# Performance work log

Hardware: AMD Instinct MI355X
Metric: run time of the kernel (lower is better)

## Reference

```python
import jax, jax.numpy as jnp
import numpy as np

G = 9.80665  # scipy.constants.g


def _xavier(key, fan_in, fan_out):
    std = np.sqrt(2.0 / (fan_in + fan_out))
    return jax.random.normal(key, (fan_in, fan_out), dtype=jnp.float32) * std


def setup_inputs() -> dict:
    key = jax.random.key(0)
    ks = jax.random.split(key, 16)
    n_samples, n_nodes, n_pipes, n_demand, hidden = 16384, 512, 1024, 256, 64
    D = jax.random.uniform(ks[0], (n_samples, n_demand), dtype=jnp.float32) * 0.01
    leak_id = jax.random.randint(ks[1], (n_samples, 1), 0, n_pipes)
    A0 = jax.random.normal(ks[2], (n_nodes, n_pipes), dtype=jnp.float32) * 0.1
    inv = jax.random.normal(ks[3], (n_nodes, n_pipes), dtype=jnp.float32) * 0.1
    M = jax.random.normal(ks[4], (n_nodes, n_pipes), dtype=jnp.float32) * 0.1
    supply = jax.random.uniform(ks[5], (n_pipes,), dtype=jnp.float32) * 10.0
    L = jax.random.uniform(ks[6], (n_pipes,), dtype=jnp.float32) * 900.0 + 100.0  # pipe length [m]
    d = jax.random.uniform(ks[7], (n_pipes,), dtype=jnp.float32) * 0.4 + 0.1      # diameter [m]
    C = jax.random.uniform(ks[8], (n_pipes,), dtype=jnp.float32) * 50.0 + 100.0   # HW coefficient
    demand_idx = jnp.arange(n_demand) * 2  # distinct node indices < n_nodes
    a = jnp.float32(0.01)   # leak area
    Cd = jnp.float32(0.75)  # discharge coefficient
    W1 = _xavier(ks[9], 1, hidden); b1 = jnp.zeros((hidden,), jnp.float32)
    W2 = _xavier(ks[10], hidden, hidden); b2 = jnp.zeros((hidden,), jnp.float32)
    W3 = _xavier(ks[11], hidden, 1); b3 = jnp.zeros((1,), jnp.float32)
    base = jax.random.normal(ks[12], (n_pipes,), dtype=jnp.float32) * 0.1
    return {"D": D, "leak_id": leak_id, "A0": A0, "inv": inv, "M": M,
            "supply": supply, "L": L, "d": d, "C": C, "a": a, "Cd": Cd,
            "W1": W1, "b1": b1, "W2": W2, "b2": b2, "W3": W3, "b3": b3,
            "base": base, "demand_idx": demand_idx}


def reference(D, leak_id, A0, inv, M, supply, L, d, C, a, Cd,
              W1, b1, W2, b2, W3, b3, base, demand_idx):
    S = D.shape[0]
    n_nodes, n_pipes = M.shape
    idx = leak_id[:, 0]  # [S] int, pipe index per sample

    # Net(leak_id): tanh MLP + lookup of per-pipe base value
    x = leak_id.astype(jnp.float32)                      # [S,1]
    h = jnp.tanh(x @ W1 + b1)
    h = jnp.tanh(h @ W2 + b2)
    net_out = base[idx][:, None] + (h @ W3 + b3)          # [S,1]

    # scatter-built demand / leakage / areas
    demand = jnp.zeros((S, n_nodes), jnp.float32).at[:, demand_idx].set(D)
    rows = jnp.arange(S)
    leakage = jnp.zeros((S, n_pipes), jnp.float32).at[rows, idx].set(net_out[:, 0])
    areas = jnp.zeros((S, n_pipes), jnp.float32).at[rows, idx].set(a)

    # q = inv.T @ (M @ leakage + demand)
    y = jnp.einsum('np,sp->sn', M, leakage) + demand      # [S,Nn]
    q = jnp.einsum('np,sn->sp', inv, y)                   # [S,Np]

    # Hazen-Williams head loss
    hL = jnp.sign(q) * 10.667 * C[None] ** (-1.852) * d[None] ** (-4.871) * L[None] * jnp.abs(q) ** 1.852
    H = jnp.einsum('np,sp->sn', inv, supply[None] - hL)   # [S,Nn]

    # leak demand d_leak = Cd * (M @ areas) * sqrt(2 g relu(H))  (safe sqrt)
    Hp = jax.nn.relu(H)
    sq = jnp.sqrt(jnp.where(Hp > 0, Hp, 1.0)) * (Hp > 0).astype(jnp.float32)
    d_leak = Cd * jnp.einsum('np,sp->sn', M, areas) * jnp.sqrt(jnp.float32(2.0 * G)) * sq

    residual = jnp.einsum('np,sp->sn', A0, q) - demand - d_leak
    return jnp.mean(residual ** 2)
```

## Files before the change

kernel.cpp:

```cpp
#include <hip/hip_runtime.h>
#include <math.h>

typedef _Float16 f16;
typedef _Float16 f16x4 __attribute__((ext_vector_type(4)));
typedef _Float16 f16x8 __attribute__((ext_vector_type(8)));
typedef float f32x4 __attribute__((ext_vector_type(4)));

#define S_TOTAL 16384
#define N_NODES 512
#define N_PIPES 1024
#define N_DEM   256
#define HIDDEN  64
#define T_SCALE 256.0f

#define GLOAD16(gsrc, ldst) \
    __builtin_amdgcn_global_load_lds((const __attribute__((address_space(1))) void*)(gsrc), \
                                     (__attribute__((address_space(3))) void*)(ldst), 16, 0, 0)
#define SBAR()  __builtin_amdgcn_s_barrier()
#define FENCE() asm volatile("" ::: "memory")
#define WAITN(n) asm volatile("s_waitcnt vmcnt(" #n ")" ::: "memory")

__global__ __launch_bounds__(256) void prep_all(
    const float* __restrict__ W1, const float* __restrict__ b1,
    const float* __restrict__ W2, const float* __restrict__ b2,
    const float* __restrict__ W3, const float* __restrict__ b3,
    const float* __restrict__ base,
    const float* __restrict__ L, const float* __restrict__ dpipe,
    const float* __restrict__ Cw,
    const float* __restrict__ Mf, const float* __restrict__ inv,
    const float* __restrict__ A0, const float* __restrict__ D,
    const int* __restrict__ dmap,
    float* __restrict__ net, float* __restrict__ lKc,
    f16* __restrict__ MT16, f16* __restrict__ invT16,
    f16* __restrict__ inv16, f16* __restrict__ A016, f16* __restrict__ D16,
    f16* __restrict__ DI16, f16* __restrict__ IDXT,
    float* __restrict__ out, int out_size)
{
    __shared__ __align__(16) f16 tile[64][72];
    const int b = blockIdx.x, t = threadIdx.x;
    if (b < 256) {
        if (b == 0) for (int i = t; i < out_size; i += 256) out[i] = 0.f;
        const int wid = t >> 6, k = t & 63;
        const int p = b * 4 + wid;
        const float x = (float)p;
        float h1 = tanhf(x * W1[k] + b1[k]);
        float acc = b2[k];
        #pragma unroll
        for (int j = 0; j < HIDDEN; ++j) {
            float hj = __shfl(h1, j, 64);
            acc = fmaf(hj, W2[j * HIDDEN + k], acc);
        }
        float partial = tanhf(acc) * W3[k];
        #pragma unroll
        for (int off = 32; off > 0; off >>= 1) partial += __shfl_down(partial, off, 64);
        if (k == 0) {
            net[p] = base[p] + partial + b3[0];
            lKc[p] = log2f(10.667f) - 1.852f * log2f(Cw[p]) - 4.871f * log2f(dpipe[p]) + log2f(L[p]);
        }
        return;
    }
    if (b < 512) {
        const int idx = b - 256;
        const float* in = (idx < 128) ? Mf : inv;
        f16* outp = (idx < 128) ? MT16 : invT16;
        const int i2 = idx & 127;
        const int bx = i2 & 15, by = i2 >> 4;
        const int r0 = by * 64, c0 = bx * 64;
        const int lr = t / 16, lc4 = (t % 16) * 4;
        #pragma unroll
        for (int i = 0; i < 4; ++i) {
            int r = lr + i * 16;
            float4 v = *(const float4*)(in + (size_t)(r0 + r) * N_PIPES + c0 + lc4);
            tile[lc4 + 0][r] = (f16)v.x; tile[lc4 + 1][r] = (f16)v.y;
            tile[lc4 + 2][r] = (f16)v.z; tile[lc4 + 3][r] = (f16)v.w;
        }
        __syncthreads();
        const int wrow = t / 4, wc16 = (t % 4) * 16;
        *(f16x8*)(outp + (size_t)(c0 + wrow) * N_NODES + r0 + wc16)     = *(f16x8*)&tile[wrow][wc16];
        *(f16x8*)(outp + (size_t)(c0 + wrow) * N_NODES + r0 + wc16 + 8) = *(f16x8*)&tile[wrow][wc16 + 8];
        return;
    }
    const int tid = (b - 512) * 256 + t;
    const int np = 768 * 256;
    for (int i = tid; i < (N_NODES * N_PIPES) / 4; i += np) {
        float4 v = ((const float4*)inv)[i];
        ((f16x4*)inv16)[i] = (f16x4){(f16)v.x, (f16)v.y, (f16)v.z, (f16)v.w};
        float4 w = ((const float4*)A0)[i];
        ((f16x4*)A016)[i] = (f16x4){(f16)w.x, (f16)w.y, (f16)w.z, (f16)w.w};
    }
    for (int i = tid; i < (S_TOTAL * N_DEM) / 4; i += np) {
        float4 v = ((const float4*)D)[i];
        ((f16x4*)D16)[i] = (f16x4){(f16)v.x, (f16)v.y, (f16)v.z, (f16)v.w};
    }
    for (int i = tid; i < N_DEM * (N_PIPES / 4); i += np) {
        int j = i >> 8, p0 = (i & 255) * 4;
        float4 v = *(const float4*)(inv + (size_t)dmap[j] * N_PIPES + p0);
        *(f16x4*)(DI16 + (size_t)j * N_PIPES + p0) = (f16x4){(f16)v.x, (f16)v.y, (f16)v.z, (f16)v.w};
    }
    for (int i = tid; i < N_PIPES * (N_DEM / 4); i += np) {
        int p = i >> 6, j0 = (i & 63) * 4;
        f16x4 o;
        #pragma unroll
        for (int u = 0; u < 4; ++u)
            o[u] = (f16)inv[(size_t)dmap[j0 + u] * N_PIPES + p];
        *(f16x4*)(IDXT + (size_t)p * N_DEM + j0) = o;
    }
}

struct GemmP {
    const f16* A; int lda;
    const f16* B; int ldb;
    f16* C; int ldc;
    int K;
    const int* dmap;
    int gx, gy;
};

__device__ __forceinline__ void gemm_body(const GemmP& P, int bx, int by) {
    __shared__ __align__(16) f16 As[128][72], Bs[64][72];
    const int m0 = by * 128, c0 = bx * 64;
    const int t = threadIdx.x, lane = t & 63, wid = t >> 6;
    const int wr = wid >> 1, wc = wid & 1;
    const int cl = lane & 15, g = lane >> 4;
    const int tr = t >> 3, tc = (t & 7) * 8;
    f32x4 acc[4][2] = {};
    for (int k0 = 0; k0 < P.K; k0 += 64) {
        #pragma unroll
        for (int r = 0; r < 4; ++r) {
            int row = r * 32 + tr;
            *(f16x8*)&As[row][tc] = *(const f16x8*)(P.A + (size_t)(m0 + row) * P.lda + k0 + tc);
        }
        #pragma unroll
        for (int r = 0; r < 2; ++r) {
            int row = r * 32 + tr;
            *(f16x8*)&Bs[row][tc] = *(const f16x8*)(P.B + (size_t)(c0 + row) * P.ldb + k0 + tc);
        }
        __syncthreads();
        #pragma unroll
        for (int kk = 0; kk < 2; ++kk) {
            const int kb = kk * 32 + g * 8;
            f16x8 a[4], bfr[2];
            #pragma unroll
            for (int m = 0; m < 4; ++m) a[m] = *(const f16x8*)&As[wr * 64 + m * 16 + cl][kb];
            #pragma unroll
            for (int n = 0; n < 2; ++n) bfr[n] = *(const f16x8*)&Bs[wc * 32 + n * 16 + cl][kb];
            #pragma unroll
            for (int m = 0; m < 4; ++m)
                #pragma unroll
                for (int n = 0; n < 2; ++n)
                    acc[m][n] = __builtin_amdgcn_mfma_f32_16x16x32_f16(a[m], bfr[n], acc[m][n], 0, 0, 0);
        }
        __syncthreads();
    }
    #pragma unroll
    for (int m = 0; m < 4; ++m)
        #pragma unroll
        for (int reg = 0; reg < 4; ++reg) {
            const int row = m0 + wr * 64 + m * 16 + g * 4 + reg;
            #pragma unroll
            for (int n = 0; n < 2; ++n) {
                const int col = c0 + wc * 32 + n * 16 + cl;
                float v = acc[m][n][reg];
                if (P.dmap && P.dmap[col] == row) v -= 1.0f;
                P.C[(size_t)row * P.ldc + col] = (f16)v;
            }
        }
}

__global__ __launch_bounds__(256) void gemm_small3(GemmP p0, GemmP p1, GemmP p2) {
    const GemmP& P = (blockIdx.z == 0) ? p0 : (blockIdx.z == 1) ? p1 : p2;
    if ((int)blockIdx.x >= P.gx || (int)blockIdx.y >= P.gy) return;
    gemm_body(P, blockIdx.x, blockIdx.y);
}

__global__ __launch_bounds__(512, 4) void gemm_qt_mfma(
    const f16* __restrict__ D16, const int* __restrict__ leak_id,
    const f16* __restrict__ IDXT, const float* __restrict__ net,
    const f16* __restrict__ G16, const float* __restrict__ lKc,
    const float* __restrict__ supply, f16* __restrict__ t16,
    const f16* __restrict__ MT16, const f16* __restrict__ Wt,
    f16* __restrict__ G2out)
{
    __shared__ __align__(16) f16 As[2][128][64];
    __shared__ __align__(16) f16 Bs[2][128][64];
    const int t = threadIdx.x, lane = t & 63, wid = t >> 6;

    if (blockIdx.y >= 128) {
        f16 (*A2)[72] = (f16(*)[72])&Bs[0][0][0];
        f16 (*B2)[72] = (f16(*)[72])&As[0][0][0];
        const int m0 = ((int)blockIdx.y - 128) * 128, c0 = blockIdx.x * 64;
        const int wr = wid >> 2, wc = wid & 3;
        const int cl = lane & 15, g = lane >> 4;
        f32x4 acc[4] = {};
        for (int k0 = 0; k0 < 512; k0 += 64) {
            {
                int r = t >> 2, c16 = (t & 3) * 16;
                *(f16x8*)&A2[r][c16]     = *(const f16x8*)(MT16 + (size_t)(m0 + r) * N_NODES + k0 + c16);
                *(f16x8*)&A2[r][c16 + 8] = *(const f16x8*)(MT16 + (size_t)(m0 + r) * N_NODES + k0 + c16 + 8);
                int r2 = t >> 3, c8 = (t & 7) * 8;
                *(f16x8*)&B2[r2][c8] = *(const f16x8*)(Wt + (size_t)(c0 + r2) * N_NODES + k0 + c8);
            }
            __syncthreads();
            #pragma unroll
            for (int kk = 0; kk < 2; ++kk) {
                const int kb = kk * 32 + g * 8;
                f16x8 b = *(const f16x8*)&B2[wc * 16 + cl][kb];
                #pragma unroll
                for (int m = 0; m < 4; ++m) {
                    f16x8 a = *(const f16x8*)&A2[wr * 64 + m * 16 + cl][kb];
                    acc[m] = __builtin_amdgcn_mfma_f32_16x16x32_f16(a, b, acc[m], 0, 0, 0);
                }
            }
            __syncthreads();
        }
        #pragma unroll
        for (int m = 0; m < 4; ++m)
            #pragma unroll
            for (int reg = 0; reg < 4; ++reg)
                G2out[(size_t)(m0 + wr * 64 + m * 16 + g * 4 + reg) * N_NODES + c0 + wc * 16 + cl] = (f16)acc[m][reg];
        return;
    }
    const int bid = blockIdx.y * 8 + blockIdx.x;
    const int w = (bid & 7) * 128 + (bid >> 3);
    const int bx = w & 7, by = w >> 3;
    const int p0 = bx * 128, sb = by * 128;
    const int wr = wid >> 2, wc = wid & 3;
    const int cl = lane & 15, g = lane >> 4;
    const int swrow = lane >> 3;
    const int swcol = ((lane & 7) ^ swrow) * 8;
    const int sx0 = (g ^ (cl & 7)) * 8, sx1 = ((4 + g) ^ (cl & 7)) * 8;

    const f16* Abase = D16 + (size_t)(sb + swrow) * N_DEM + swcol;
    const f16* Bbase = IDXT + (size_t)(p0 + swrow) * N_DEM + swcol;

    f32x4 acc[4][2] = {};
    auto stage = [&](int buf, int k0) {
        #pragma unroll
        for (int c = 0; c < 2; ++c) {
            int r0 = c * 64 + wid * 8;
            GLOAD16(Abase + (size_t)r0 * N_DEM + k0, &As[buf][r0][0]);
        }
        #pragma unroll
        for (int c = 0; c < 2; ++c) {
            int r0 = c * 64 + wid * 8;
            GLOAD16(Bbase + (size_t)r0 * N_DEM + k0, &Bs[buf][r0][0]);
        }
    };
    auto compute = [&](int buf) {
        #pragma unroll
        for (int kk = 0; kk < 2; ++kk) {
            const int sx = kk ? sx1 : sx0;
            f16x8 a[4], b[2];
            #pragma unroll
            for (int m = 0; m < 4; ++m) a[m] = *(const f16x8*)&As[buf][wr * 64 + m * 16 + cl][sx];
            #pragma unroll
            for (int n = 0; n < 2; ++n) b[n] = *(const f16x8*)&Bs[buf][wc * 32 + n * 16 + cl][sx];
            #pragma unroll
            for (int m = 0; m < 4; ++m)
                #pragma unroll
                for (int n = 0; n < 2; ++n)
                    acc[m][n] = __builtin_amdgcn_mfma_f32_16x16x32_f16(a[m], b[n], acc[m][n], 0, 0, 0);
        }
    };

    int cur = 0;
    stage(0, 0);
    #pragma unroll 1
    for (int k = 0; k < 3; ++k) {
        stage(cur ^ 1, (k + 1) * 64);
        WAITN(4); SBAR();
        compute(cur);
        FENCE(); SBAR();
        cur ^= 1;
    }
    WAITN(0); SBAR();
    compute(cur);

    float lKc2[2], sup2[2]; int pcol[2];
    #pragma unroll
    for (int n = 0; n < 2; ++n) {
        pcol[n] = p0 + wc * 32 + n * 16 + cl;
        lKc2[n] = lKc[pcol[n]]; sup2[n] = supply[pcol[n]];
    }
    #pragma unroll
    for (int m = 0; m < 4; ++m) {
        #pragma unroll
        for (int reg = 0; reg < 4; ++reg) {
            const int srow = sb + wr * 64 + m * 16 + g * 4 + reg;
            const int idx = leak_id[srow];
            const float nv = net[idx];
            #pragma unroll
            for (int n = 0; n < 2; ++n) {
                float qv = acc[m][n][reg] + nv * (float)G16[(size_t)idx * N_PIPES + pcol[n]];
                float l = __builtin_amdgcn_logf(fabsf(qv));
                float hL = copysignf(__builtin_amdgcn_exp2f(fmaf(1.852f, l, lKc2[n])), qv);
                t16[(size_t)srow * N_PIPES + pcol[n]] = (f16)((sup2[n] - hL) * (1.0f / T_SCALE));
            }
        }
    }
}

__global__ __launch_bounds__(512, 4) void gemm_res_mfma(
    const f16* __restrict__ t16, const f16* __restrict__ inv16,
    const f16* __restrict__ D16, const f16* __restrict__ P1p,
    const f16* __restrict__ MT16, const f16* __restrict__ G2_16,
    const int* __restrict__ leak_id, const float* __restrict__ net,
    const float* __restrict__ Cd_p, const float* __restrict__ a_p,
    float scale, float* __restrict__ out)
{
    __shared__ __align__(16) f16 As[2][128][64];
    __shared__ __align__(16) f16 Bs[2][128][64];
    const int nwg = gridDim.x * gridDim.y;
    const int bid = blockIdx.y * gridDim.x + blockIdx.x;
    const int w = (bid & 7) * (nwg >> 3) + (bid >> 3);
    const int bx = w % gridDim.x, by = w / gridDim.x;
    const int n0 = bx * 128, sb = by * 128;
    const int t = threadIdx.x, lane = t & 63, wid = t >> 6;
    const int wr = wid >> 2, wc = wid & 3;
    const int cl = lane & 15, g = lane >> 4;
    const int swrow = lane >> 3;
    const int swcol = ((lane & 7) ^ swrow) * 8;
    const int sx0 = (g ^ (cl & 7)) * 8, sx1 = ((4 + g) ^ (cl & 7)) * 8;

    const f16* HAb = t16   + (size_t)(sb + swrow) * N_PIPES + swcol;
    const f16* HBb = inv16 + (size_t)(n0 + swrow) * N_PIPES + swcol;
    const f16* RAb = D16   + (size_t)(sb + swrow) * N_DEM + swcol;
    const f16* RBb = P1p   + (size_t)(n0 + swrow) * N_DEM + swcol;

    f32x4 accH[4][2] = {}, accR[4][2] = {};

    auto stageH = [&](int buf, int k0) {
        #pragma unroll
        for (int c = 0; c < 2; ++c) {
            int r0 = c * 64 + wid * 8;
            GLOAD16(HAb + (size_t)r0 * N_PIPES + k0, &As[buf][r0][0]);
        }
        #pragma unroll
        for (int c = 0; c < 2; ++c) {
            int r0 = c * 64 + wid * 8;
            GLOAD16(HBb + (size_t)r0 * N_PIPES + k0, &Bs[buf][r0][0]);
        }
    };
    auto stageR = [&](int buf, int k0) {
        #pragma unroll
        for (int c = 0; c < 2; ++c) {
            int r0 = c * 64 + wid * 8;
            GLOAD16(RAb + (size_t)r0 * N_DEM + k0, &As[buf][r0][0]);
        }
        #pragma unroll
        for (int c = 0; c < 2; ++c) {
            int r0 = c * 64 + wid * 8;
            GLOAD16(RBb + (size_t)r0 * N_DEM + k0, &Bs[buf][r0][0]);
        }
    };
    auto computeT = [&](int buf, f32x4 (&accA)[4][2]) {
        #pragma unroll
        for (int kk = 0; kk < 2; ++kk) {
            const int sx = kk ? sx1 : sx0;
            f16x8 a[4], b[2];
            #pragma unroll
            for (int m = 0; m < 4; ++m) a[m] = *(const f16x8*)&As[buf][wr * 64 + m * 16 + cl][sx];
            #pragma unroll
            for (int n = 0; n < 2; ++n) b[n] = *(const f16x8*)&Bs[buf][wc * 32 + n * 16 + cl][sx];
            #pragma unroll
            for (int m = 0; m < 4; ++m)
                #pragma unroll
                for (int n = 0; n < 2; ++n)
                    accA[m][n] = __builtin_amdgcn_mfma_f32_16x16x32_f16(a[m], b[n], accA[m][n], 0, 0, 0);
        }
    };

    int cur = 0;
    stageH(0, 0);
    #pragma unroll 1
    for (int k = 0; k < 15; ++k) {
        stageH(cur ^ 1, (k + 1) * 64);
        WAITN(4); SBAR();
        computeT(cur, accH);
        FENCE(); SBAR();
        cur ^= 1;
    }
    stageR(cur ^ 1, 0);
    WAITN(4); SBAR();
    computeT(cur, accH);
    FENCE(); SBAR();
    cur ^= 1;
    #pragma unroll 1
    for (int k = 0; k < 3; ++k) {
        stageR(cur ^ 1, (k + 1) * 64);
        WAITN(4); SBAR();
        computeT(cur, accR);
        FENCE(); SBAR();
        cur ^= 1;
    }
    WAITN(0); SBAR();
    computeT(cur, accR);

    const float cda = Cd_p[0] * a_p[0] * sqrtf(2.f * 9.80665f);
    int node[2];
    #pragma unroll
    for (int n = 0; n < 2; ++n) node[n] = n0 + wc * 32 + n * 16 + cl;
    float lsum = 0.f;
    #pragma unroll
    for (int m = 0; m < 4; ++m) {
        #pragma unroll
        for (int reg = 0; reg < 4; ++reg) {
            const int srow = sb + wr * 64 + m * 16 + g * 4 + reg;
            const int idx = leak_id[srow];
            const float nv = net[idx];
            #pragma unroll
            for (int n = 0; n < 2; ++n) {
                const float H = accH[m][n][reg] * T_SCALE;
                const float sq = (H > 0.f) ? sqrtf(H) : 0.f;
                const float dl = cda * (float)MT16[(size_t)idx * N_NODES + node[n]] * sq;
                const float r = accR[m][n][reg] + nv * (float)G2_16[(size_t)idx * N_NODES + node[n]] - dl;
                lsum += r * r;
            }
        }
    }
    #pragma unroll
    for (int off = 32; off > 0; off >>= 1) lsum += __shfl_down(lsum, off, 64);
    __syncthreads();
    float* wred = (float*)&As[0][0][0];
    if (lane == 0) wred[wid] = lsum;
    __syncthreads();
    if (t == 0) {
        float tot = 0.f;
        #pragma unroll
        for (int i = 0; i < 8; ++i) tot += wred[i];
        atomicAdd(out, tot * scale);
    }
}

extern "C" void kernel_launch(void* const* d_in, const int* in_sizes, int n_in,
                              void* d_out, int out_size, void* d_ws, size_t ws_size,
                              hipStream_t stream) {
    const float* D          = (const float*)d_in[0];
    const int*   leak_id    = (const int*)  d_in[1];
    const float* A0         = (const float*)d_in[2];
    const float* inv        = (const float*)d_in[3];
    const float* M          = (const float*)d_in[4];
    const float* supply     = (const float*)d_in[5];
    const float* L          = (const float*)d_in[6];
    const float* dpipe      = (const float*)d_in[7];
    const float* C          = (const float*)d_in[8];
    const float* a_p        = (const float*)d_in[9];
    const float* Cd_p       = (const float*)d_in[10];
    const float* W1         = (const float*)d_in[11];
    const float* b1         = (const float*)d_in[12];
    const float* W2         = (const float*)d_in[13];
    const float* b2         = (const float*)d_in[14];
    const float* W3         = (const float*)d_in[15];
    const float* b3         = (const float*)d_in[16];
    const float* base       = (const float*)d_in[17];
    const int*   demand_idx = (const int*)  d_in[18];

    char* ws = (char*)d_ws;
    size_t off = 0;
    auto carve = [&](size_t bytes) { char* p = ws + off; off += (bytes + 255) & ~(size_t)255; return p; };
    float* net    = (float*)carve(N_PIPES * 4);
    float* lKc    = (float*)carve(N_PIPES * 4);
    f16* inv16  = (f16*)carve((size_t)N_NODES * N_PIPES * 2);
    f16* A016   = (f16*)carve((size_t)N_NODES * N_PIPES * 2);
    f16* MT16   = (f16*)carve((size_t)N_PIPES * N_NODES * 2);
    f16* invT16 = (f16*)carve((size_t)N_PIPES * N_NODES * 2);
    f16* G16    = (f16*)carve((size_t)N_PIPES * N_PIPES * 2);
    f16* G2_16  = (f16*)carve((size_t)N_PIPES * N_NODES * 2);
    f16* Wt     = (f16*)carve((size_t)N_NODES * N_NODES * 2);
    f16* P1p    = (f16*)carve((size_t)N_NODES * N_DEM * 2);
    f16* DI16   = (f16*)carve((size_t)N_DEM * N_PIPES * 2);
    f16* IDXT   = (f16*)carve((size_t)N_PIPES * N_DEM * 2);
    f16* D16    = (f16*)carve((size_t)S_TOTAL * N_DEM * 2);
    f16* t16    = (f16*)carve((size_t)S_TOTAL * N_PIPES * 2);

    prep_all<<<1280, 256, 0, stream>>>(
        W1, b1, W2, b2, W3, b3, base, L, dpipe, C,
        M, inv, A0, D, demand_idx,
        net, lKc, MT16, invT16, inv16, A016, D16, DI16, IDXT,
        (float*)d_out, out_size);

    GemmP pG16 = {MT16, N_NODES, invT16, N_NODES, G16, N_PIPES, N_NODES, nullptr, 16, 8};
    GemmP pWt  = {A016, N_PIPES, inv16, N_PIPES, Wt, N_NODES, N_PIPES, nullptr, 8, 4};
    GemmP pP1  = {A016, N_PIPES, DI16, N_PIPES, P1p, N_DEM, N_PIPES, demand_idx, 4, 4};
    gemm_small3<<<dim3(16, 8, 3), 256, 0, stream>>>(pG16, pWt, pP1);

    gemm_qt_mfma<<<dim3(8, 136), 512, 0, stream>>>(
        D16, leak_id, IDXT, net, G16, lKc, supply, t16, MT16, Wt, G2_16);

    const float scale = 1.f / ((float)S_TOTAL * (float)N_NODES);
    gemm_res_mfma<<<dim3(N_NODES / 128, S_TOTAL / 128), 512, 0, stream>>>(
        t16, inv16, D16, P1p, MT16, G2_16, leak_id, net, Cd_p, a_p,
        scale, (float*)d_out);
}
```

Measured before the change: 94.47 us.

## Store head-loss intermediate and inv in bf8 and use bf8 MFMA for H GEMM

The per-sample head-loss tensor t and the inv matrix are now quantized to 8-bit bf8 (e5m2) instead of f16. The H GEMM in the residual kernel uses 16x16x32 bf8 MFMA with 128-wide K tiles and a new LDS swizzle, halving the number of K iterations. This halves the bytes written and read for the large S x N_pipes intermediate and doubles MFMA throughput. The cost is a large loss of precision (2-bit mantissa) in H, which risks exceeding the correctness tolerance.

```diff
diff --git a/kernel.cpp b/kernel.cpp
--- a/kernel.cpp
+++ b/kernel.cpp
@@ -19,6 +19,12 @@
 #define SBAR()  __builtin_amdgcn_s_barrier()
 #define FENCE() asm volatile("" ::: "memory")
 #define WAITN(n) asm volatile("s_waitcnt vmcnt(" #n ")" ::: "memory")
+
+__device__ __forceinline__ unsigned char f32_to_bf8(float x) {
+    unsigned short h = __builtin_bit_cast(unsigned short, (f16)x);
+    unsigned short r = (unsigned short)(h + 0x7F + ((h >> 8) & 1));
+    return (unsigned char)(r >> 8);
+}
 
 __global__ __launch_bounds__(256) void prep_all(
     const float* __restrict__ W1, const float* __restrict__ b1,
@@ -32,7 +38,8 @@
     const int* __restrict__ dmap,
     float* __restrict__ net, float* __restrict__ lKc,
     f16* __restrict__ MT16, f16* __restrict__ invT16,
-    f16* __restrict__ inv16, f16* __restrict__ A016, f16* __restrict__ D16,
+    f16* __restrict__ inv16, unsigned char* __restrict__ inv8,
+    f16* __restrict__ A016, f16* __restrict__ D16,
     f16* __restrict__ DI16, f16* __restrict__ IDXT,
     float* __restrict__ out, int out_size)
 {
@@ -85,6 +92,8 @@
     for (int i = tid; i < (N_NODES * N_PIPES) / 4; i += np) {
         float4 v = ((const float4*)inv)[i];
         ((f16x4*)inv16)[i] = (f16x4){(f16)v.x, (f16)v.y, (f16)v.z, (f16)v.w};
+        uchar4 v8 = {f32_to_bf8(v.x), f32_to_bf8(v.y), f32_to_bf8(v.z), f32_to_bf8(v.w)};
+        ((uchar4*)inv8)[i] = v8;
         float4 w = ((const float4*)A0)[i];
         ((f16x4*)A016)[i] = (f16x4){(f16)w.x, (f16)w.y, (f16)w.z, (f16)w.w};
     }
@@ -177,7 +186,7 @@
     const f16* __restrict__ D16, const int* __restrict__ leak_id,
     const f16* __restrict__ IDXT, const float* __restrict__ net,
     const f16* __restrict__ G16, const float* __restrict__ lKc,
-    const float* __restrict__ supply, f16* __restrict__ t16,
+    const float* __restrict__ supply, unsigned char* __restrict__ t8,
     const f16* __restrict__ MT16, const f16* __restrict__ Wt,
     f16* __restrict__ G2out)
 {
@@ -294,22 +303,22 @@
                 float qv = acc[m][n][reg] + nv * (float)G16[(size_t)idx * N_PIPES + pcol[n]];
                 float l = __builtin_amdgcn_logf(fabsf(qv));
                 float hL = copysignf(__builtin_amdgcn_exp2f(fmaf(1.852f, l, lKc2[n])), qv);
-                t16[(size_t)srow * N_PIPES + pcol[n]] = (f16)((sup2[n] - hL) * (1.0f / T_SCALE));
+                t8[(size_t)srow * N_PIPES + pcol[n]] = f32_to_bf8((sup2[n] - hL) * (1.0f / T_SCALE));
             }
         }
     }
 }
 
 __global__ __launch_bounds__(512, 4) void gemm_res_mfma(
-    const f16* __restrict__ t16, const f16* __restrict__ inv16,
+    const unsigned char* __restrict__ t8, const unsigned char* __restrict__ inv8,
     const f16* __restrict__ D16, const f16* __restrict__ P1p,
     const f16* __restrict__ MT16, const f16* __restrict__ G2_16,
     const int* __restrict__ leak_id, const float* __restrict__ net,
     const float* __restrict__ Cd_p, const float* __restrict__ a_p,
     float scale, float* __restrict__ out)
 {
-    __shared__ __align__(16) f16 As[2][128][64];
-    __shared__ __align__(16) f16 Bs[2][128][64];
+    __shared__ __align__(16) unsigned char AsM[2][128 * 128];
+    __shared__ __align__(16) unsigned char BsM[2][128 * 128];
     const int nwg = gridDim.x * gridDim.y;
     const int bid = blockIdx.y * gridDim.x + blockIdx.x;
     const int w = (bid & 7) * (nwg >> 3) + (bid >> 3);
@@ -319,82 +328,103 @@
     const int wr = wid >> 2, wc = wid & 3;
     const int cl = lane & 15, g = lane >> 4;
     const int swrow = lane >> 3;
-    const int swcol = ((lane & 7) ^ swrow) * 8;
-    const int sx0 = (g ^ (cl & 7)) * 8, sx1 = ((4 + g) ^ (cl & 7)) * 8;
-
-    const f16* HAb = t16   + (size_t)(sb + swrow) * N_PIPES + swcol;
-    const f16* HBb = inv16 + (size_t)(n0 + swrow) * N_PIPES + swcol;
-    const f16* RAb = D16   + (size_t)(sb + swrow) * N_DEM + swcol;
-    const f16* RBb = P1p   + (size_t)(n0 + swrow) * N_DEM + swcol;
+    const int swb = ((lane & 7) ^ swrow) * 16;
+
+    const unsigned char* HAb = t8   + (size_t)(sb + swrow) * N_PIPES + swb;
+    const unsigned char* HBb = inv8 + (size_t)(n0 + swrow) * N_PIPES + swb;
+    const f16* RAb = D16 + (size_t)(sb + swrow) * N_DEM + swb / 2;
+    const f16* RBb = P1p + (size_t)(n0 + swrow) * N_DEM + swb / 2;
 
     f32x4 accH[4][2] = {}, accR[4][2] = {};
 
     auto stageH = [&](int buf, int k0) {
+        #pragma unroll
+        for (int c = 0; c < 2; ++c) {
+            int r0 = wid * 16 + c * 8;
+            GLOAD16(HAb + (size_t)r0 * N_PIPES + k0, &AsM[buf][r0 * 128]);
+        }
+        #pragma unroll
+        for (int c = 0; c < 2; ++c) {
+            int r0 = wid * 16 + c * 8;
+            GLOAD16(HBb + (size_t)r0 * N_PIPES + k0, &BsM[buf][r0 * 128]);
+        }
+    };
+    auto computeH = [&](int buf) {
+        #pragma unroll
+        for (int ks = 0; ks < 4; ++ks) {
+            const int bo = (ks * 32 + g * 8) ^ ((cl & 7) << 4);
+            long long a[4], b[2];
+            #pragma unroll
+            for (int m = 0; m < 4; ++m)
+                a[m] = *(const long long*)&AsM[buf][(wr * 64 + m * 16 + cl) * 128 + bo];
+            #pragma unroll
+            for (int n = 0; n < 2; ++n)
+                b[n] = *(const long long*)&BsM[buf][(wc * 32 + n * 16 + cl) * 128 + bo];
+            #pragma unroll
+            for (int m = 0; m < 4; ++m)
+                #pragma unroll
+                for (int n = 0; n < 2; ++n)
+                    accH[m][n] = __builtin_amdgcn_mfma_f32_16x16x32_bf8_bf8(a[m], b[n], accH[m][n], 0, 0, 0);
+        }
+    };
+
+    f16 (*AsF)[128 * 64] = (f16(*)[128 * 64])AsM;
+    f16 (*BsF)[128 * 64] = (f16(*)[128 * 64])BsM;
+    auto stageR = [&](int buf, int k0) {
         #pragma unroll
         for (int c = 0; c < 2; ++c) {
             int r0 = c * 64 + wid * 8;
-            GLOAD16(HAb + (size_t)r0 * N_PIPES + k0, &As[buf][r0][0]);
+            GLOAD16(RAb + (size_t)r0 * N_DEM + k0, &AsF[buf][r0 * 64]);
         }
         #pragma unroll
         for (int c = 0; c < 2; ++c) {
             int r0 = c * 64 + wid * 8;
-            GLOAD16(HBb + (size_t)r0 * N_PIPES + k0, &Bs[buf][r0][0]);
+            GLOAD16(RBb + (size_t)r0 * N_DEM + k0, &BsF[buf][r0 * 64]);
         }
     };
-    auto stageR = [&](int buf, int k0) {
-        #pragma unroll
-        for (int c = 0; c < 2; ++c) {
-            int r0 = c * 64 + wid * 8;
-            GLOAD16(RAb + (size_t)r0 * N_DEM + k0, &As[buf][r0][0]);
-        }
-        #pragma unroll
-        for (int c = 0; c < 2; ++c) {
-            int r0 = c * 64 + wid * 8;
-            GLOAD16(RBb + (size_t)r0 * N_DEM + k0, &Bs[buf][r0][0]);
-        }
-    };
-    auto computeT = [&](int buf, f32x4 (&accA)[4][2]) {
+    const int sx0 = (g ^ (cl & 7)) * 8, sx1 = ((4 + g) ^ (cl & 7)) * 8;
+    auto computeR = [&](int buf) {
         #pragma unroll
         for (int kk = 0; kk < 2; ++kk) {
             const int sx = kk ? sx1 : sx0;
             f16x8 a[4], b[2];
             #pragma unroll
-            for (int m = 0; m < 4; ++m) a[m] = *(const f16x8*)&As[buf][wr * 64 + m * 16 + cl][sx];
-            #pragma unroll
-            for (int n = 0; n < 2; ++n) b[n] = *(const f16x8*)&Bs[buf][wc * 32 + n * 16 + cl][sx];
+            for (int m = 0; m < 4; ++m) a[m] = *(const f16x8*)&AsF[buf][(wr * 64 + m * 16 + cl) * 64 + sx];
+            #pragma unroll
+            for (int n = 0; n < 2; ++n) b[n] = *(const f16x8*)&BsF[buf][(wc * 32 + n * 16 + cl) * 64 + sx];
             #pragma unroll
             for (int m = 0; m < 4; ++m)
                 #pragma unroll
                 for (int n = 0; n < 2; ++n)
-                    accA[m][n] = __builtin_amdgcn_mfma_f32_16x16x32_f16(a[m], b[n], accA[m][n], 0, 0, 0);
+                    accR[m][n] = __builtin_amdgcn_mfma_f32_16x16x32_f16(a[m], b[n], accR[m][n], 0, 0, 0);
         }
     };
 
     int cur = 0;
     stageH(0, 0);
     #pragma unroll 1
-    for (int k = 0; k < 15; ++k) {
-        stageH(cur ^ 1, (k + 1) * 64);
+    for (int k = 0; k < 7; ++k) {
+        stageH(cur ^ 1, (k + 1) * 128);
         WAITN(4); SBAR();
-        computeT(cur, accH);
+        computeH(cur);
         FENCE(); SBAR();
         cur ^= 1;
     }
     stageR(cur ^ 1, 0);
     WAITN(4); SBAR();
-    computeT(cur, accH);
+    computeH(cur);
     FENCE(); SBAR();
     cur ^= 1;
     #pragma unroll 1
     for (int k = 0; k < 3; ++k) {
         stageR(cur ^ 1, (k + 1) * 64);
         WAITN(4); SBAR();
-        computeT(cur, accR);
+        computeR(cur);
         FENCE(); SBAR();
         cur ^= 1;
     }
     WAITN(0); SBAR();
-    computeT(cur, accR);
+    computeR(cur);
 
     const float cda = Cd_p[0] * a_p[0] * sqrtf(2.f * 9.80665f);
     int node[2];
@@ -421,7 +451,7 @@
     #pragma unroll
     for (int off = 32; off > 0; off >>= 1) lsum += __shfl_down(lsum, off, 64);
     __syncthreads();
-    float* wred = (float*)&As[0][0][0];
+    float* wred = (float*)&AsM[0][0];
     if (lane == 0) wred[wid] = lsum;
     __syncthreads();
     if (t == 0) {
@@ -461,6 +491,7 @@
     float* net    = (float*)carve(N_PIPES * 4);
     float* lKc    = (float*)carve(N_PIPES * 4);
     f16* inv16  = (f16*)carve((size_t)N_NODES * N_PIPES * 2);
+    unsigned char* inv8 = (unsigned char*)carve((size_t)N_NODES * N_PIPES);
     f16* A016   = (f16*)carve((size_t)N_NODES * N_PIPES * 2);
     f16* MT16   = (f16*)carve((size_t)N_PIPES * N_NODES * 2);
     f16* invT16 = (f16*)carve((size_t)N_PIPES * N_NODES * 2);
@@ -471,12 +502,12 @@
     f16* DI16   = (f16*)carve((size_t)N_DEM * N_PIPES * 2);
     f16* IDXT   = (f16*)carve((size_t)N_PIPES * N_DEM * 2);
     f16* D16    = (f16*)carve((size_t)S_TOTAL * N_DEM * 2);
-    f16* t16    = (f16*)carve((size_t)S_TOTAL * N_PIPES * 2);
+    unsigned char* t8 = (unsigned char*)carve((size_t)S_TOTAL * N_PIPES);
 
     prep_all<<<1280, 256, 0, stream>>>(
         W1, b1, W2, b2, W3, b3, base, L, dpipe, C,
         M, inv, A0, D, demand_idx,
-        net, lKc, MT16, invT16, inv16, A016, D16, DI16, IDXT,
+        net, lKc, MT16, invT16, inv16, inv8, A016, D16, DI16, IDXT,
         (float*)d_out, out_size);
 
     GemmP pG16 = {MT16, N_NODES, invT16, N_NODES, G16, N_PIPES, N_NODES, nullptr, 16, 8};
@@ -485,10 +516,10 @@
     gemm_small3<<<dim3(16, 8, 3), 256, 0, stream>>>(pG16, pWt, pP1);
 
     gemm_qt_mfma<<<dim3(8, 136), 512, 0, stream>>>(
-        D16, leak_id, IDXT, net, G16, lKc, supply, t16, MT16, Wt, G2_16);
+        D16, leak_id, IDXT, net, G16, lKc, supply, t8, MT16, Wt, G2_16);
 
     const float scale = 1.f / ((float)S_TOTAL * (float)N_NODES);
     gemm_res_mfma<<<dim3(N_NODES / 128, S_TOTAL / 128), 512, 0, stream>>>(
-        t16, inv16, D16, P1p, MT16, G2_16, leak_id, net, Cd_p, a_p,
+        t8, inv8, D16, P1p, MT16, G2_16, leak_id, net, Cd_p, a_p,
         scale, (float*)d_out);
 }
```

After: 89.59 us. -5.2%, faster.
